# Performance work log

Hardware: AMD Instinct MI355X
Metric: run time of the kernel (lower is better)

Reference implementation:

```python
import jax, jax.numpy as jnp
import numpy as np

B, T, D, H, C = 64, 1024, 128, 512, 2


def setup_inputs() -> dict:
    key = jax.random.key(0)
    ks = jax.random.split(key, 6)
    x = jax.random.normal(ks[0], (B, T, D), dtype=jnp.float32)
    labels = jax.random.randint(ks[1], (B, T), 0, C, dtype=jnp.int32)
    # Keras LSTMCell params: kernel [D,4H], recurrent_kernel [H,4H], bias [4H]
    Wx = jax.random.normal(ks[2], (D, 4 * H), dtype=jnp.float32) * (1.0 / np.sqrt(D))
    Wh = jax.random.normal(ks[3], (H, 4 * H), dtype=jnp.float32) * (1.0 / np.sqrt(H))
    b = jnp.zeros((4 * H,), dtype=jnp.float32).at[H:2 * H].set(1.0)  # unit forget bias
    Wo = jax.random.normal(ks[4], (H, C), dtype=jnp.float32) * (1.0 / np.sqrt(H))
    bo = jnp.zeros((C,), dtype=jnp.float32)
    return {"x": x, "labels": labels, "Wx": Wx, "Wh": Wh, "b": b, "Wo": Wo, "bo": bo}


def _lstm_logits(x, Wx, Wh, b, Wo, bo):
    # Precompute input contribution for all steps: [B,T,4H]
    xz = jnp.einsum('btd,dk->btk', x, Wx) + b

    def step(carry, z_t):
        h, c = carry
        z = z_t + h @ Wh                     # [B,4H]
        i, f, g, o = jnp.split(z, 4, axis=-1)  # keras gate order: i,f,c,o
        i = jax.nn.sigmoid(i)
        f = jax.nn.sigmoid(f)
        g = jnp.tanh(g)
        o = jax.nn.sigmoid(o)
        c = f * c + i * g
        h = o * jnp.tanh(c)
        return (h, c), h

    h0 = jnp.zeros((x.shape[0], Wh.shape[0]), dtype=x.dtype)
    (_, _), hs = jax.lax.scan(step, (h0, h0), jnp.swapaxes(xz, 0, 1))
    hs = jnp.swapaxes(hs, 0, 1)              # [B,T,H]
    return jnp.einsum('bth,hc->btc', hs, Wo) + bo  # [B,T,C]


def reference(x, labels, Wx, Wh, b, Wo, bo):
    logits = _lstm_logits(x, Wx, Wh, b, Wo, bo)
    logp = jax.nn.log_softmax(logits, axis=-1)
    prediction = jnp.exp(logp)               # softmax probs
    nll = -jnp.take_along_axis(logp, labels[..., None].astype(jnp.int32), axis=-1)[..., 0]
    cost = jnp.mean(nll)
    return prediction, cost
```

## Files before the change

kernel.cpp:

```cpp
#include <hip/hip_runtime.h>
#include <stdint.h>

#define TLEN 1024
#define BATCH 64
#define DIMX 128
#define HID 512

typedef __attribute__((ext_vector_type(8))) short short8;
typedef __attribute__((ext_vector_type(4))) float f32x4;
typedef __attribute__((ext_vector_type(4))) unsigned u32x4;

#define OFF_WT   0u
#define OFF_XBF  2621440u
#define OFF_HB   19398656u
#define OFF_ACC  19660800u
#define ZERO_LEN (262144u + 64u)

__device__ __forceinline__ unsigned short f2bf(float f) {
  unsigned u = __float_as_uint(f);
  u += 0x7fffu + ((u >> 16) & 1u);
  return (unsigned short)(u >> 16);
}
__device__ __forceinline__ float sigm(float x) { return 1.0f / (1.0f + __expf(-x)); }
__device__ __forceinline__ float tanh_fast(float x) {
  float a = fabsf(x);
  float e = __expf(2.0f * a);
  float t = 1.0f - 2.0f / (e + 1.0f);
  return copysignf(t, x);
}

__global__ void k_convx(const float4* __restrict__ x4, ushort4* __restrict__ o4) {
  int i = blockIdx.x * 256 + threadIdx.x;
  float4 v = x4[i];
  ushort4 o;
  o.x = f2bf(v.x); o.y = f2bf(v.y); o.z = f2bf(v.z); o.w = f2bf(v.w);
  o4[i] = o;
}

__global__ void k_tw(const float* __restrict__ Wx, const float* __restrict__ Wh,
                     unsigned short* __restrict__ Wt) {
  __shared__ float tile[32][65];
  int bk = blockIdx.x;
  int k0 = (bk / 64) * 64;
  int c0 = (bk % 64) * 32;
  int tid = threadIdx.x;
  const float* src = (k0 < 128) ? (Wx + (size_t)k0 * 2048)
                                : (Wh + (size_t)(k0 - 128) * 2048);
#pragma unroll
  for (int p = 0; p < 8; ++p) {
    int i = p * 256 + tid;
    int kk = i >> 5, cc = i & 31;
    tile[cc][kk] = src[(size_t)kk * 2048 + (c0 + cc)];
  }
  __syncthreads();
  int cc = tid >> 3, ch = tid & 7;
  unsigned short tmp[8];
#pragma unroll
  for (int j = 0; j < 8; ++j) tmp[j] = f2bf(tile[cc][ch * 8 + j]);
  uint4 o;
  o.x = (unsigned)tmp[0] | ((unsigned)tmp[1] << 16);
  o.y = (unsigned)tmp[2] | ((unsigned)tmp[3] << 16);
  o.z = (unsigned)tmp[4] | ((unsigned)tmp[5] << 16);
  o.w = (unsigned)tmp[6] | ((unsigned)tmp[7] << 16);
  *(uint4*)(Wt + (size_t)(c0 + cc) * 640 + k0 + ch * 8) = o;
}

__global__ __launch_bounds__(512, 1) void k_lstm(
    const unsigned short* __restrict__ xbf,
    const unsigned short* __restrict__ Wt,
    const float* __restrict__ bias,
    const float* __restrict__ Wo,
    unsigned* __restrict__ hb,
    float* __restrict__ out)
{
  __shared__ float red[2][4][4][8][32];

  const int tid  = threadIdx.x;
  const int w    = tid >> 6;
  const int kw   = w & 3;
  const int cg   = w >> 2;
  const int lane = tid & 63;
  const int q    = lane >> 4;
  const int m    = lane & 15;
  const int grp  = blockIdx.x & 7;
  const int hj   = blockIdx.x >> 3;
  const int g0   = grp * 8;

  short8 Bf[5][4];
#pragma unroll
  for (int cc = 0; cc < 5; ++cc) {
#pragma unroll
    for (int j = 0; j < 4; ++j) {
      int gate = cg * 2 + (j >> 1);
      int col = gate * HID + hj * 32 + (j & 1) * 16 + m;
      int k = (cc == 0) ? (kw * 32 + q * 8)
                        : (128 + kw * 128 + (cc - 1) * 32 + q * 8);
      Bf[cc][j] = *(const short8*)(Wt + (size_t)col * 640 + k);
    }
  }

  const int row = tid >> 5;
  const int col = tid & 31;
  const int hcol = hj * 32 + col;
  float c_state = 0.0f;
  float b_i = 0, b_f = 0, b_g = 0, b_o = 0;
  float2 wo = {0.f, 0.f};
  if (tid < 256) {
    b_i = bias[0 * HID + hcol];
    b_f = bias[1 * HID + hcol];
    b_g = bias[2 * HID + hcol];
    b_o = bias[3 * HID + hcol];
    wo = ((const float2*)Wo)[hcol];
  }

  const int arow = (m < 8) ? m : 7;
  const int ab = g0 + arow;

#pragma unroll 1
  for (int t = 0; t < TLEN; ++t) {
    const unsigned* hin = hb + (size_t)(t & 1) * (BATCH * HID);

    short8 a0 = *(const short8*)(xbf + ((size_t)ab * TLEN + t) * DIMX +
                                 kw * 32 + q * 8);

    const unsigned* pb = hin + (size_t)ab * HID + kw * 128 + q * 8;
    u32x4 r0, r1, r2, r3, r4, r5, r6, r7;
    {
      const unsigned tg = (unsigned)t & 0xFFFFu;
      int guard = 0;
      for (;;) {
        asm volatile(
            "global_load_dwordx4 %0, %8, off sc0 sc1\n\t"
            "global_load_dwordx4 %1, %8, off offset:16 sc0 sc1\n\t"
            "global_load_dwordx4 %2, %8, off offset:128 sc0 sc1\n\t"
            "global_load_dwordx4 %3, %8, off offset:144 sc0 sc1\n\t"
            "global_load_dwordx4 %4, %8, off offset:256 sc0 sc1\n\t"
            "global_load_dwordx4 %5, %8, off offset:272 sc0 sc1\n\t"
            "global_load_dwordx4 %6, %8, off offset:384 sc0 sc1\n\t"
            "global_load_dwordx4 %7, %8, off offset:400 sc0 sc1\n\t"
            "s_waitcnt vmcnt(0)"
            : "=v"(r0), "=v"(r1), "=v"(r2), "=v"(r3),
              "=v"(r4), "=v"(r5), "=v"(r6), "=v"(r7)
            : "v"(pb)
            : "memory");
        unsigned d = (r0[0] ^ tg) | (r0[1] ^ tg) | (r0[2] ^ tg) | (r0[3] ^ tg);
        d |= (r1[0] ^ tg) | (r1[1] ^ tg) | (r1[2] ^ tg) | (r1[3] ^ tg);
        d |= (r2[0] ^ tg) | (r2[1] ^ tg) | (r2[2] ^ tg) | (r2[3] ^ tg);
        d |= (r3[0] ^ tg) | (r3[1] ^ tg) | (r3[2] ^ tg) | (r3[3] ^ tg);
        d |= (r4[0] ^ tg) | (r4[1] ^ tg) | (r4[2] ^ tg) | (r4[3] ^ tg);
        d |= (r5[0] ^ tg) | (r5[1] ^ tg) | (r5[2] ^ tg) | (r5[3] ^ tg);
        d |= (r6[0] ^ tg) | (r6[1] ^ tg) | (r6[2] ^ tg) | (r6[3] ^ tg);
        d |= (r7[0] ^ tg) | (r7[1] ^ tg) | (r7[2] ^ tg) | (r7[3] ^ tg);
        bool bad = (d & 0xFFFFu) != 0u;
        if (__ballot(bad) == 0ull || ++guard > (1 << 20)) break;
      }
    }

    short8 a[5];
    a[0] = a0;
    {
      union { short8 s; unsigned u[4]; } pk;
#define PACK(dst, RA, RB)                                            \
      pk.u[0] = (RA[0] >> 16) | (RA[1] & 0xFFFF0000u);               \
      pk.u[1] = (RA[2] >> 16) | (RA[3] & 0xFFFF0000u);               \
      pk.u[2] = (RB[0] >> 16) | (RB[1] & 0xFFFF0000u);               \
      pk.u[3] = (RB[2] >> 16) | (RB[3] & 0xFFFF0000u);               \
      dst = pk.s;
      PACK(a[1], r0, r1)
      PACK(a[2], r2, r3)
      PACK(a[3], r4, r5)
      PACK(a[4], r6, r7)
#undef PACK
    }

    f32x4 z0 = {0,0,0,0}, z1 = {0,0,0,0}, z2 = {0,0,0,0}, z3 = {0,0,0,0};
#pragma unroll
    for (int cc = 0; cc < 5; ++cc) {
      z0 = __builtin_amdgcn_mfma_f32_16x16x32_bf16(a[cc], Bf[cc][0], z0, 0, 0, 0);
      z1 = __builtin_amdgcn_mfma_f32_16x16x32_bf16(a[cc], Bf[cc][1], z1, 0, 0, 0);
      z2 = __builtin_amdgcn_mfma_f32_16x16x32_bf16(a[cc], Bf[cc][2], z2, 0, 0, 0);
      z3 = __builtin_amdgcn_mfma_f32_16x16x32_bf16(a[cc], Bf[cc][3], z3, 0, 0, 0);
    }

    const int buf = t & 1;
    if (q < 2) {
#pragma unroll
      for (int r = 0; r < 4; ++r) {
        int rw = q * 4 + r;
        red[buf][kw][cg * 2 + 0][rw][0 * 16 + m] = z0[r];
        red[buf][kw][cg * 2 + 0][rw][1 * 16 + m] = z1[r];
        red[buf][kw][cg * 2 + 1][rw][0 * 16 + m] = z2[r];
        red[buf][kw][cg * 2 + 1][rw][1 * 16 + m] = z3[r];
      }
    }
    __syncthreads();

    if (tid < 256) {
      float zi = b_i + red[buf][0][0][row][col] + red[buf][1][0][row][col]
                     + red[buf][2][0][row][col] + red[buf][3][0][row][col];
      float zf = b_f + red[buf][0][1][row][col] + red[buf][1][1][row][col]
                     + red[buf][2][1][row][col] + red[buf][3][1][row][col];
      float zg = b_g + red[buf][0][2][row][col] + red[buf][1][2][row][col]
                     + red[buf][2][2][row][col] + red[buf][3][2][row][col];
      float zo = b_o + red[buf][0][3][row][col] + red[buf][1][3][row][col]
                     + red[buf][2][3][row][col] + red[buf][3][3][row][col];
      float ig = sigm(zi), fg = sigm(zf), gg = tanh_fast(zg), og = sigm(zo);
      c_state = fg * c_state + ig * gg;
      float hval = og * tanh_fast(c_state);

      unsigned hword = ((unsigned)f2bf(hval) << 16) | (unsigned)((t + 1) & 0xFFFF);
      __hip_atomic_store(hb + (size_t)((t + 1) & 1) * (BATCH * HID) +
                             (size_t)(g0 + row) * HID + hcol,
                         hword, __ATOMIC_RELAXED, __HIP_MEMORY_SCOPE_AGENT);

      float p0 = hval * wo.x, p1 = hval * wo.y;
      p0 += __shfl_xor(p0, 16); p1 += __shfl_xor(p1, 16);
      p0 += __shfl_xor(p0, 8);  p1 += __shfl_xor(p1, 8);
      p0 += __shfl_xor(p0, 4);  p1 += __shfl_xor(p1, 4);
      p0 += __shfl_xor(p0, 2);  p1 += __shfl_xor(p1, 2);
      p0 += __shfl_xor(p0, 1);  p1 += __shfl_xor(p1, 1);
      if (col == 0) {
        float* po = out + ((size_t)(g0 + row) * TLEN + t) * 2;
        atomicAdd(po + 0, p0);
        atomicAdd(po + 1, p1);
      }
    }
  }
}

__global__ void k_out2(float* __restrict__ out, const float* __restrict__ bo,
                       const int* __restrict__ labels, float* __restrict__ acc) {
  __shared__ float sred[4];
  int i = blockIdx.x * 256 + threadIdx.x;
  float l0 = out[(size_t)i * 2 + 0] + bo[0];
  float l1 = out[(size_t)i * 2 + 1] + bo[1];
  float mx = fmaxf(l0, l1);
  float e0 = __expf(l0 - mx), e1 = __expf(l1 - mx);
  float s = e0 + e1, inv = 1.0f / s;
  out[(size_t)i * 2 + 0] = e0 * inv;
  out[(size_t)i * 2 + 1] = e1 * inv;
  int lab = labels[i];
  float nll = __logf(s) - ((lab ? l1 : l0) - mx);
#pragma unroll
  for (int off = 32; off >= 1; off >>= 1) nll += __shfl_xor(nll, off);
  if ((threadIdx.x & 63) == 0) sred[threadIdx.x >> 6] = nll;
  __syncthreads();
  if (threadIdx.x == 0)
    atomicAdd(acc, sred[0] + sred[1] + sred[2] + sred[3]);
}

__global__ void k_fin(const float* __restrict__ acc, float* __restrict__ out) {
  out[BATCH * TLEN * 2] = acc[0] * (1.0f / (float)(BATCH * TLEN));
}

extern "C" void kernel_launch(void* const* d_in, const int* in_sizes, int n_in,
                              void* d_out, int out_size, void* d_ws, size_t ws_size,
                              hipStream_t stream) {
  const float* x      = (const float*)d_in[0];
  const int*   labels = (const int*)d_in[1];
  const float* Wx     = (const float*)d_in[2];
  const float* Wh     = (const float*)d_in[3];
  const float* b      = (const float*)d_in[4];
  const float* Wo     = (const float*)d_in[5];
  const float* bo     = (const float*)d_in[6];
  float* out = (float*)d_out;
  char* ws = (char*)d_ws;

  unsigned short* Wt  = (unsigned short*)(ws + OFF_WT);
  unsigned short* xbf = (unsigned short*)(ws + OFF_XBF);
  unsigned*       hb  = (unsigned*)(ws + OFF_HB);
  float*          acc = (float*)(ws + OFF_ACC);

  hipMemsetAsync(ws + OFF_HB, 0, ZERO_LEN, stream);
  hipMemsetAsync(d_out, 0, (size_t)BATCH * TLEN * 2 * sizeof(float), stream);
  k_convx<<<8192, 256, 0, stream>>>((const float4*)x, (ushort4*)xbf);
  k_tw<<<640, 256, 0, stream>>>(Wx, Wh, Wt);
  k_lstm<<<128, 512, 0, stream>>>(xbf, Wt, b, Wo, hb, out);
  k_out2<<<256, 256, 0, stream>>>(out, bo, labels, acc);
  k_fin<<<1, 1, 0, stream>>>(acc, out);
}
```

Measured before the change: 3.300 ms.

## Split recurrent h polling across wave pairs with LDS exchange and vectorized h stores

Each wave pair that shares a k-slice now polls only half of the recurrent h data from global memory and swaps the other half through shared memory, guarded by per-step LDS flags. The gate epilogue is spread across all eight waves, one batch row per wave, instead of four. Each wave packs its h words into dwordx4 stores through shuffles rather than issuing scalar atomic stores. The aim is to cut global polling traffic and store count on the latency-bound recurrence step, at the cost of an extra intra-block spin handshake that could add latency or stall.

After: 2.785 ms. -15.6%, faster.

```diff
diff --git a/kernel.cpp b/kernel.cpp
--- a/kernel.cpp
+++ b/kernel.cpp
@@ -74,6 +74,8 @@
     float* __restrict__ out)
 {
   __shared__ float red[2][4][4][8][32];
+  __shared__ short8 xch[2][4][2][2][64];
+  __shared__ unsigned xflag[2][4][2];
 
   const int tid  = threadIdx.x;
   const int w    = tid >> 6;
@@ -86,6 +88,8 @@
   const int hj   = blockIdx.x >> 3;
   const int g0   = grp * 8;
 
+  if (tid < 16) xflag[tid >> 3][(tid >> 1) & 3][tid & 1] = 0;
+
   short8 Bf[5][4];
 #pragma unroll
   for (int cc = 0; cc < 5; ++cc) {
@@ -99,90 +103,108 @@
     }
   }
 
-  const int row = tid >> 5;
-  const int col = tid & 31;
+  const int col  = lane & 31;
   const int hcol = hj * 32 + col;
   float c_state = 0.0f;
-  float b_i = 0, b_f = 0, b_g = 0, b_o = 0;
-  float2 wo = {0.f, 0.f};
-  if (tid < 256) {
-    b_i = bias[0 * HID + hcol];
-    b_f = bias[1 * HID + hcol];
-    b_g = bias[2 * HID + hcol];
-    b_o = bias[3 * HID + hcol];
-    wo = ((const float2*)Wo)[hcol];
-  }
+  const float b_i = bias[0 * HID + hcol];
+  const float b_f = bias[1 * HID + hcol];
+  const float b_g = bias[2 * HID + hcol];
+  const float b_o = bias[3 * HID + hcol];
+  const float2 wo = ((const float2*)Wo)[hcol];
 
   const int arow = (m < 8) ? m : 7;
   const int ab = g0 + arow;
+
+  __syncthreads();
 
 #pragma unroll 1
   for (int t = 0; t < TLEN; ++t) {
     const unsigned* hin = hb + (size_t)(t & 1) * (BATCH * HID);
+    const int buf = t & 1;
 
     short8 a0 = *(const short8*)(xbf + ((size_t)ab * TLEN + t) * DIMX +
                                  kw * 32 + q * 8);
 
-    const unsigned* pb = hin + (size_t)ab * HID + kw * 128 + q * 8;
-    u32x4 r0, r1, r2, r3, r4, r5, r6, r7;
+    const unsigned* pb = hin + (size_t)ab * HID + kw * 128 + cg * 64 + q * 8;
+    u32x4 r0, r1, r2, r3;
     {
       const unsigned tg = (unsigned)t & 0xFFFFu;
       int guard = 0;
       for (;;) {
         asm volatile(
-            "global_load_dwordx4 %0, %8, off sc0 sc1\n\t"
-            "global_load_dwordx4 %1, %8, off offset:16 sc0 sc1\n\t"
-            "global_load_dwordx4 %2, %8, off offset:128 sc0 sc1\n\t"
-            "global_load_dwordx4 %3, %8, off offset:144 sc0 sc1\n\t"
-            "global_load_dwordx4 %4, %8, off offset:256 sc0 sc1\n\t"
-            "global_load_dwordx4 %5, %8, off offset:272 sc0 sc1\n\t"
-            "global_load_dwordx4 %6, %8, off offset:384 sc0 sc1\n\t"
-            "global_load_dwordx4 %7, %8, off offset:400 sc0 sc1\n\t"
+            "global_load_dwordx4 %0, %4, off sc0 sc1\n\t"
+            "global_load_dwordx4 %1, %4, off offset:16 sc0 sc1\n\t"
+            "global_load_dwordx4 %2, %4, off offset:128 sc0 sc1\n\t"
+            "global_load_dwordx4 %3, %4, off offset:144 sc0 sc1\n\t"
             "s_waitcnt vmcnt(0)"
-            : "=v"(r0), "=v"(r1), "=v"(r2), "=v"(r3),
-              "=v"(r4), "=v"(r5), "=v"(r6), "=v"(r7)
+            : "=v"(r0), "=v"(r1), "=v"(r2), "=v"(r3)
             : "v"(pb)
             : "memory");
         unsigned d = (r0[0] ^ tg) | (r0[1] ^ tg) | (r0[2] ^ tg) | (r0[3] ^ tg);
         d |= (r1[0] ^ tg) | (r1[1] ^ tg) | (r1[2] ^ tg) | (r1[3] ^ tg);
         d |= (r2[0] ^ tg) | (r2[1] ^ tg) | (r2[2] ^ tg) | (r2[3] ^ tg);
         d |= (r3[0] ^ tg) | (r3[1] ^ tg) | (r3[2] ^ tg) | (r3[3] ^ tg);
-        d |= (r4[0] ^ tg) | (r4[1] ^ tg) | (r4[2] ^ tg) | (r4[3] ^ tg);
-        d |= (r5[0] ^ tg) | (r5[1] ^ tg) | (r5[2] ^ tg) | (r5[3] ^ tg);
-        d |= (r6[0] ^ tg) | (r6[1] ^ tg) | (r6[2] ^ tg) | (r6[3] ^ tg);
-        d |= (r7[0] ^ tg) | (r7[1] ^ tg) | (r7[2] ^ tg) | (r7[3] ^ tg);
         bool bad = (d & 0xFFFFu) != 0u;
         if (__ballot(bad) == 0ull || ++guard > (1 << 20)) break;
       }
     }
 
-    short8 a[5];
-    a[0] = a0;
+    short8 f0, f1;
     {
       union { short8 s; unsigned u[4]; } pk;
-#define PACK(dst, RA, RB)                                            \
-      pk.u[0] = (RA[0] >> 16) | (RA[1] & 0xFFFF0000u);               \
-      pk.u[1] = (RA[2] >> 16) | (RA[3] & 0xFFFF0000u);               \
-      pk.u[2] = (RB[0] >> 16) | (RB[1] & 0xFFFF0000u);               \
-      pk.u[3] = (RB[2] >> 16) | (RB[3] & 0xFFFF0000u);               \
-      dst = pk.s;
-      PACK(a[1], r0, r1)
-      PACK(a[2], r2, r3)
-      PACK(a[3], r4, r5)
-      PACK(a[4], r6, r7)
-#undef PACK
-    }
+      pk.u[0] = (r0[0] >> 16) | (r0[1] & 0xFFFF0000u);
+      pk.u[1] = (r0[2] >> 16) | (r0[3] & 0xFFFF0000u);
+      pk.u[2] = (r1[0] >> 16) | (r1[1] & 0xFFFF0000u);
+      pk.u[3] = (r1[2] >> 16) | (r1[3] & 0xFFFF0000u);
+      f0 = pk.s;
+      pk.u[0] = (r2[0] >> 16) | (r2[1] & 0xFFFF0000u);
+      pk.u[1] = (r2[2] >> 16) | (r2[3] & 0xFFFF0000u);
+      pk.u[2] = (r3[0] >> 16) | (r3[1] & 0xFFFF0000u);
+      pk.u[3] = (r3[2] >> 16) | (r3[3] & 0xFFFF0000u);
+      f1 = pk.s;
+    }
+
+    xch[buf][kw][cg][0][lane] = f0;
+    xch[buf][kw][cg][1][lane] = f1;
+    __hip_atomic_store(&xflag[buf][kw][cg], (unsigned)(t + 1),
+                       __ATOMIC_RELEASE, __HIP_MEMORY_SCOPE_WORKGROUP);
+    {
+      int guard = 0;
+      while (__hip_atomic_load(&xflag[buf][kw][cg ^ 1], __ATOMIC_ACQUIRE,
+                               __HIP_MEMORY_SCOPE_WORKGROUP) < (unsigned)(t + 1)) {
+        if (++guard > (1 << 22)) break;
+      }
+    }
+    short8 s0 = xch[buf][kw][cg ^ 1][0][lane];
+    short8 s1 = xch[buf][kw][cg ^ 1][1][lane];
+
+    short8 a1 = cg ? s0 : f0;
+    short8 a2 = cg ? s1 : f1;
+    short8 a3 = cg ? f0 : s0;
+    short8 a4 = cg ? f1 : s1;
 
     f32x4 z0 = {0,0,0,0}, z1 = {0,0,0,0}, z2 = {0,0,0,0}, z3 = {0,0,0,0};
-#pragma unroll
-    for (int cc = 0; cc < 5; ++cc) {
-      z0 = __builtin_amdgcn_mfma_f32_16x16x32_bf16(a[cc], Bf[cc][0], z0, 0, 0, 0);
-      z1 = __builtin_amdgcn_mfma_f32_16x16x32_bf16(a[cc], Bf[cc][1], z1, 0, 0, 0);
-      z2 = __builtin_amdgcn_mfma_f32_16x16x32_bf16(a[cc], Bf[cc][2], z2, 0, 0, 0);
-      z3 = __builtin_amdgcn_mfma_f32_16x16x32_bf16(a[cc], Bf[cc][3], z3, 0, 0, 0);
-    }
-
-    const int buf = t & 1;
+    z0 = __builtin_amdgcn_mfma_f32_16x16x32_bf16(a0, Bf[0][0], z0, 0, 0, 0);
+    z1 = __builtin_amdgcn_mfma_f32_16x16x32_bf16(a0, Bf[0][1], z1, 0, 0, 0);
+    z2 = __builtin_amdgcn_mfma_f32_16x16x32_bf16(a0, Bf[0][2], z2, 0, 0, 0);
+    z3 = __builtin_amdgcn_mfma_f32_16x16x32_bf16(a0, Bf[0][3], z3, 0, 0, 0);
+    z0 = __builtin_amdgcn_mfma_f32_16x16x32_bf16(a1, Bf[1][0], z0, 0, 0, 0);
+    z1 = __builtin_amdgcn_mfma_f32_16x16x32_bf16(a1, Bf[1][1], z1, 0, 0, 0);
+    z2 = __builtin_amdgcn_mfma_f32_16x16x32_bf16(a1, Bf[1][2], z2, 0, 0, 0);
+    z3 = __builtin_amdgcn_mfma_f32_16x16x32_bf16(a1, Bf[1][3], z3, 0, 0, 0);
+    z0 = __builtin_amdgcn_mfma_f32_16x16x32_bf16(a2, Bf[2][0], z0, 0, 0, 0);
+    z1 = __builtin_amdgcn_mfma_f32_16x16x32_bf16(a2, Bf[2][1], z1, 0, 0, 0);
+    z2 = __builtin_amdgcn_mfma_f32_16x16x32_bf16(a2, Bf[2][2], z2, 0, 0, 0);
+    z3 = __builtin_amdgcn_mfma_f32_16x16x32_bf16(a2, Bf[2][3], z3, 0, 0, 0);
+    z0 = __builtin_amdgcn_mfma_f32_16x16x32_bf16(a3, Bf[3][0], z0, 0, 0, 0);
+    z1 = __builtin_amdgcn_mfma_f32_16x16x32_bf16(a3, Bf[3][1], z1, 0, 0, 0);
+    z2 = __builtin_amdgcn_mfma_f32_16x16x32_bf16(a3, Bf[3][2], z2, 0, 0, 0);
+    z3 = __builtin_amdgcn_mfma_f32_16x16x32_bf16(a3, Bf[3][3], z3, 0, 0, 0);
+    z0 = __builtin_amdgcn_mfma_f32_16x16x32_bf16(a4, Bf[4][0], z0, 0, 0, 0);
+    z1 = __builtin_amdgcn_mfma_f32_16x16x32_bf16(a4, Bf[4][1], z1, 0, 0, 0);
+    z2 = __builtin_amdgcn_mfma_f32_16x16x32_bf16(a4, Bf[4][2], z2, 0, 0, 0);
+    z3 = __builtin_amdgcn_mfma_f32_16x16x32_bf16(a4, Bf[4][3], z3, 0, 0, 0);
+
     if (q < 2) {
 #pragma unroll
       for (int r = 0; r < 4; ++r) {
@@ -195,23 +217,32 @@
     }
     __syncthreads();
 
-    if (tid < 256) {
-      float zi = b_i + red[buf][0][0][row][col] + red[buf][1][0][row][col]
-                     + red[buf][2][0][row][col] + red[buf][3][0][row][col];
-      float zf = b_f + red[buf][0][1][row][col] + red[buf][1][1][row][col]
-                     + red[buf][2][1][row][col] + red[buf][3][1][row][col];
-      float zg = b_g + red[buf][0][2][row][col] + red[buf][1][2][row][col]
-                     + red[buf][2][2][row][col] + red[buf][3][2][row][col];
-      float zo = b_o + red[buf][0][3][row][col] + red[buf][1][3][row][col]
-                     + red[buf][2][3][row][col] + red[buf][3][3][row][col];
+    if (lane < 32) {
+      float zi = b_i + red[buf][0][0][w][col] + red[buf][1][0][w][col]
+                     + red[buf][2][0][w][col] + red[buf][3][0][w][col];
+      float zf = b_f + red[buf][0][1][w][col] + red[buf][1][1][w][col]
+                     + red[buf][2][1][w][col] + red[buf][3][1][w][col];
+      float zg = b_g + red[buf][0][2][w][col] + red[buf][1][2][w][col]
+                     + red[buf][2][2][w][col] + red[buf][3][2][w][col];
+      float zo = b_o + red[buf][0][3][w][col] + red[buf][1][3][w][col]
+                     + red[buf][2][3][w][col] + red[buf][3][3][w][col];
       float ig = sigm(zi), fg = sigm(zf), gg = tanh_fast(zg), og = sigm(zo);
       c_state = fg * c_state + ig * gg;
       float hval = og * tanh_fast(c_state);
 
       unsigned hword = ((unsigned)f2bf(hval) << 16) | (unsigned)((t + 1) & 0xFFFF);
-      __hip_atomic_store(hb + (size_t)((t + 1) & 1) * (BATCH * HID) +
-                             (size_t)(g0 + row) * HID + hcol,
-                         hword, __ATOMIC_RELAXED, __HIP_MEMORY_SCOPE_AGENT);
+      int base = lane & ~3;
+      unsigned w0 = __shfl(hword, base + 0);
+      unsigned w1 = __shfl(hword, base + 1);
+      unsigned w2 = __shfl(hword, base + 2);
+      unsigned w3 = __shfl(hword, base + 3);
+      if ((lane & 3) == 0) {
+        u32x4 v4 = {w0, w1, w2, w3};
+        unsigned* dst = hb + (size_t)((t + 1) & 1) * (BATCH * HID) +
+                        (size_t)(g0 + w) * HID + hcol;
+        asm volatile("global_store_dwordx4 %0, %1, off sc0 sc1"
+                     :: "v"(dst), "v"(v4) : "memory");
+      }
 
       float p0 = hval * wo.x, p1 = hval * wo.y;
       p0 += __shfl_xor(p0, 16); p1 += __shfl_xor(p1, 16);
@@ -219,8 +250,8 @@
       p0 += __shfl_xor(p0, 4);  p1 += __shfl_xor(p1, 4);
       p0 += __shfl_xor(p0, 2);  p1 += __shfl_xor(p1, 2);
       p0 += __shfl_xor(p0, 1);  p1 += __shfl_xor(p1, 1);
-      if (col == 0) {
-        float* po = out + ((size_t)(g0 + row) * TLEN + t) * 2;
+      if (lane == 0) {
+        float* po = out + ((size_t)(g0 + w) * TLEN + t) * 2;
         atomicAdd(po + 0, p0);
         atomicAdd(po + 1, p1);
       }
```

## Halve LSTM block count by giving each wave all four gates and wider columns

Applied to the files above, without the earlier changes.

The recurrent kernel now launches 64 blocks of 256 threads instead of 128 blocks of 512. Each wave keeps all four gates for 64 hidden columns in registers and issues 16 MFMAs per k-chunk instead of 4. The shared-memory reduction layout now packs the four gates as a float4, so each thread produces two hidden outputs with vector LDS reads. Hidden-state writes are gathered by shuffle into dwordx4 stores. The aim is to cut the number of blocks polling and publishing h each step, and to shrink the per-step sync and reduction cost. The trade-offs are much higher register pressure (80 resident B fragments plus 16 accumulators, with possible spills) and a longer serial MFMA chain per wave.

Result: slower. 4.156 ms (+25.9%).

```diff
diff --git a/kernel.cpp b/kernel.cpp
--- a/kernel.cpp
+++ b/kernel.cpp
@@ -65,7 +65,7 @@
   *(uint4*)(Wt + (size_t)(c0 + cc) * 640 + k0 + ch * 8) = o;
 }
 
-__global__ __launch_bounds__(512, 1) void k_lstm(
+__global__ __launch_bounds__(256, 1) void k_lstm(
     const unsigned short* __restrict__ xbf,
     const unsigned short* __restrict__ Wt,
     const float* __restrict__ bias,
@@ -73,12 +73,10 @@
     unsigned* __restrict__ hb,
     float* __restrict__ out)
 {
-  __shared__ float red[2][4][4][8][32];
+  __shared__ float red[2][4][4][8][16][4];
 
   const int tid  = threadIdx.x;
-  const int w    = tid >> 6;
-  const int kw   = w & 3;
-  const int cg   = w >> 2;
+  const int kw   = tid >> 6;
   const int lane = tid & 63;
   const int q    = lane >> 4;
   const int m    = lane & 15;
@@ -86,39 +84,39 @@
   const int hj   = blockIdx.x >> 3;
   const int g0   = grp * 8;
 
-  short8 Bf[5][4];
-#pragma unroll
-  for (int cc = 0; cc < 5; ++cc) {
-#pragma unroll
-    for (int j = 0; j < 4; ++j) {
-      int gate = cg * 2 + (j >> 1);
-      int col = gate * HID + hj * 32 + (j & 1) * 16 + m;
-      int k = (cc == 0) ? (kw * 32 + q * 8)
-                        : (128 + kw * 128 + (cc - 1) * 32 + q * 8);
-      Bf[cc][j] = *(const short8*)(Wt + (size_t)col * 640 + k);
+  short8 Bf[5][16];
+#pragma unroll
+  for (int c = 0; c < 5; ++c) {
+#pragma unroll
+    for (int j = 0; j < 16; ++j) {
+      int gate = j & 3, hc4 = j >> 2;
+      int col = gate * HID + hj * 64 + hc4 * 16 + m;
+      int k = (c == 0) ? (kw * 32 + q * 8)
+                       : (128 + kw * 128 + (c - 1) * 32 + q * 8);
+      Bf[c][j] = *(const short8*)(Wt + (size_t)col * 640 + k);
     }
   }
 
-  const int row = tid >> 5;
-  const int col = tid & 31;
-  const int hcol = hj * 32 + col;
-  float c_state = 0.0f;
-  float b_i = 0, b_f = 0, b_g = 0, b_o = 0;
-  float2 wo = {0.f, 0.f};
-  if (tid < 256) {
-    b_i = bias[0 * HID + hcol];
-    b_f = bias[1 * HID + hcol];
-    b_g = bias[2 * HID + hcol];
-    b_o = bias[3 * HID + hcol];
-    wo = ((const float2*)Wo)[hcol];
-  }
-
-  const int arow = (m < 8) ? m : 7;
-  const int ab = g0 + arow;
+  const int grow = tid >> 5;
+  const int hp   = tid & 31;
+  const int hcA  = hj * 64 + hp;
+  const int hcB  = hcA + 32;
+  float cstA = 0.f, cstB = 0.f;
+  const float biA = bias[0 * HID + hcA], biB = bias[0 * HID + hcB];
+  const float bfA = bias[1 * HID + hcA], bfB = bias[1 * HID + hcB];
+  const float bgA = bias[2 * HID + hcA], bgB = bias[2 * HID + hcB];
+  const float boA = bias[3 * HID + hcA], boB = bias[3 * HID + hcB];
+  const float2 woA = ((const float2*)Wo)[hcA];
+  const float2 woB = ((const float2*)Wo)[hcB];
+  const int hc4A = hp >> 4;
+  const int mA   = hp & 15;
+
+  const int ab = g0 + (m & 7);
 
 #pragma unroll 1
   for (int t = 0; t < TLEN; ++t) {
     const unsigned* hin = hb + (size_t)(t & 1) * (BATCH * HID);
+    const int buf = t & 1;
 
     short8 a0 = *(const short8*)(xbf + ((size_t)ab * TLEN + t) * DIMX +
                                  kw * 32 + q * 8);
@@ -173,54 +171,76 @@
 #undef PACK
     }
 
-    f32x4 z0 = {0,0,0,0}, z1 = {0,0,0,0}, z2 = {0,0,0,0}, z3 = {0,0,0,0};
-#pragma unroll
-    for (int cc = 0; cc < 5; ++cc) {
-      z0 = __builtin_amdgcn_mfma_f32_16x16x32_bf16(a[cc], Bf[cc][0], z0, 0, 0, 0);
-      z1 = __builtin_amdgcn_mfma_f32_16x16x32_bf16(a[cc], Bf[cc][1], z1, 0, 0, 0);
-      z2 = __builtin_amdgcn_mfma_f32_16x16x32_bf16(a[cc], Bf[cc][2], z2, 0, 0, 0);
-      z3 = __builtin_amdgcn_mfma_f32_16x16x32_bf16(a[cc], Bf[cc][3], z3, 0, 0, 0);
-    }
-
-    const int buf = t & 1;
+    f32x4 acc[16];
+#pragma unroll
+    for (int j = 0; j < 16; ++j) acc[j] = (f32x4){0.f, 0.f, 0.f, 0.f};
+#pragma unroll
+    for (int c = 0; c < 5; ++c) {
+#pragma unroll
+      for (int j = 0; j < 16; ++j)
+        acc[j] = __builtin_amdgcn_mfma_f32_16x16x32_bf16(a[c], Bf[c][j], acc[j],
+                                                         0, 0, 0);
+    }
+
     if (q < 2) {
 #pragma unroll
-      for (int r = 0; r < 4; ++r) {
-        int rw = q * 4 + r;
-        red[buf][kw][cg * 2 + 0][rw][0 * 16 + m] = z0[r];
-        red[buf][kw][cg * 2 + 0][rw][1 * 16 + m] = z1[r];
-        red[buf][kw][cg * 2 + 1][rw][0 * 16 + m] = z2[r];
-        red[buf][kw][cg * 2 + 1][rw][1 * 16 + m] = z3[r];
+      for (int hc4 = 0; hc4 < 4; ++hc4) {
+#pragma unroll
+        for (int r = 0; r < 4; ++r) {
+          f32x4 v = {acc[hc4 * 4 + 0][r], acc[hc4 * 4 + 1][r],
+                     acc[hc4 * 4 + 2][r], acc[hc4 * 4 + 3][r]};
+          *(f32x4*)&red[buf][kw][hc4][q * 4 + r][m][0] = v;
+        }
       }
     }
     __syncthreads();
 
-    if (tid < 256) {
-      float zi = b_i + red[buf][0][0][row][col] + red[buf][1][0][row][col]
-                     + red[buf][2][0][row][col] + red[buf][3][0][row][col];
-      float zf = b_f + red[buf][0][1][row][col] + red[buf][1][1][row][col]
-                     + red[buf][2][1][row][col] + red[buf][3][1][row][col];
-      float zg = b_g + red[buf][0][2][row][col] + red[buf][1][2][row][col]
-                     + red[buf][2][2][row][col] + red[buf][3][2][row][col];
-      float zo = b_o + red[buf][0][3][row][col] + red[buf][1][3][row][col]
-                     + red[buf][2][3][row][col] + red[buf][3][3][row][col];
-      float ig = sigm(zi), fg = sigm(zf), gg = tanh_fast(zg), og = sigm(zo);
-      c_state = fg * c_state + ig * gg;
-      float hval = og * tanh_fast(c_state);
-
-      unsigned hword = ((unsigned)f2bf(hval) << 16) | (unsigned)((t + 1) & 0xFFFF);
-      __hip_atomic_store(hb + (size_t)((t + 1) & 1) * (BATCH * HID) +
-                             (size_t)(g0 + row) * HID + hcol,
-                         hword, __ATOMIC_RELAXED, __HIP_MEMORY_SCOPE_AGENT);
-
-      float p0 = hval * wo.x, p1 = hval * wo.y;
+    {
+      f32x4 zA = {biA, bfA, bgA, boA};
+      f32x4 zB = {biB, bfB, bgB, boB};
+#pragma unroll
+      for (int k2 = 0; k2 < 4; ++k2) {
+        zA += *(const f32x4*)&red[buf][k2][hc4A][grow][mA][0];
+        zB += *(const f32x4*)&red[buf][k2][hc4A + 2][grow][mA][0];
+      }
+      float igA = sigm(zA[0]), fgA = sigm(zA[1]);
+      float ggA = tanh_fast(zA[2]), ogA = sigm(zA[3]);
+      cstA = fgA * cstA + igA * ggA;
+      float hA = ogA * tanh_fast(cstA);
+      float igB = sigm(zB[0]), fgB = sigm(zB[1]);
+      float ggB = tanh_fast(zB[2]), ogB = sigm(zB[3]);
+      cstB = fgB * cstB + igB * ggB;
+      float hB = ogB * tanh_fast(cstB);
+
+      unsigned tg1 = (unsigned)((t + 1) & 0xFFFF);
+      unsigned hwA = ((unsigned)f2bf(hA) << 16) | tg1;
+      unsigned hwB = ((unsigned)f2bf(hB) << 16) | tg1;
+
+      int bse = lane & ~3;
+      unsigned a0s = __shfl(hwA, bse + 0), a1s = __shfl(hwA, bse + 1);
+      unsigned a2s = __shfl(hwA, bse + 2), a3s = __shfl(hwA, bse + 3);
+      unsigned b0s = __shfl(hwB, bse + 0), b1s = __shfl(hwB, bse + 1);
+      unsigned b2s = __shfl(hwB, bse + 2), b3s = __shfl(hwB, bse + 3);
+      if ((lane & 3) == 0) {
+        unsigned* dst = hb + (size_t)((t + 1) & 1) * (BATCH * HID) +
+                        (size_t)(g0 + grow) * HID + hcA;
+        u32x4 vA = {a0s, a1s, a2s, a3s};
+        u32x4 vB = {b0s, b1s, b2s, b3s};
+        asm volatile("global_store_dwordx4 %0, %1, off sc0 sc1"
+                     :: "v"(dst), "v"(vA) : "memory");
+        asm volatile("global_store_dwordx4 %0, %1, off sc0 sc1"
+                     :: "v"(dst + 32), "v"(vB) : "memory");
+      }
+
+      float p0 = hA * woA.x + hB * woB.x;
+      float p1 = hA * woA.y + hB * woB.y;
+      p0 += __shfl_xor(p0, 1);  p1 += __shfl_xor(p1, 1);
+      p0 += __shfl_xor(p0, 2);  p1 += __shfl_xor(p1, 2);
+      p0 += __shfl_xor(p0, 4);  p1 += __shfl_xor(p1, 4);
+      p0 += __shfl_xor(p0, 8);  p1 += __shfl_xor(p1, 8);
       p0 += __shfl_xor(p0, 16); p1 += __shfl_xor(p1, 16);
-      p0 += __shfl_xor(p0, 8);  p1 += __shfl_xor(p1, 8);
-      p0 += __shfl_xor(p0, 4);  p1 += __shfl_xor(p1, 4);
-      p0 += __shfl_xor(p0, 2);  p1 += __shfl_xor(p1, 2);
-      p0 += __shfl_xor(p0, 1);  p1 += __shfl_xor(p1, 1);
-      if (col == 0) {
-        float* po = out + ((size_t)(g0 + row) * TLEN + t) * 2;
+      if ((lane & 31) == 0) {
+        float* po = out + ((size_t)(g0 + grow) * TLEN + t) * 2;
         atomicAdd(po + 0, p0);
         atomicAdd(po + 1, p1);
       }
@@ -275,7 +295,7 @@
   hipMemsetAsync(d_out, 0, (size_t)BATCH * TLEN * 2 * sizeof(float), stream);
   k_convx<<<8192, 256, 0, stream>>>((const float4*)x, (ushort4*)xbf);
   k_tw<<<640, 256, 0, stream>>>(Wx, Wh, Wt);
-  k_lstm<<<128, 512, 0, stream>>>(xbf, Wt, b, Wo, hb, out);
+  k_lstm<<<64, 256, 0, stream>>>(xbf, Wt, b, Wo, hb, out);
   k_out2<<<256, 256, 0, stream>>>(out, bo, labels, acc);
   k_fin<<<1, 1, 0, stream>>>(acc, out);
 }
```
